# Kernel tuning notes

Hardware: AMD Instinct MI355X
Metric: run time of the kernel (lower is better)

Reference implementation:

```python
import jax, jax.numpy as jnp
import numpy as np

NLE_TERM_CO = 80
NUM_CHARS = 256
HID = 128


def setup_inputs() -> dict:
    key = jax.random.key(0)
    ks = jax.random.split(key, 9)
    B = 8192
    message = jax.random.randint(ks[0], (B, NLE_TERM_CO), 0, NUM_CHARS, dtype=jnp.int64)
    # Linear weights stored as (in, out); scaled like torch default init.
    s1 = 1.0 / np.sqrt(NLE_TERM_CO * NUM_CHARS)
    s2 = 1.0 / np.sqrt(HID)
    return {
        "message": message,
        "W1": jax.random.normal(ks[1], (NLE_TERM_CO * NUM_CHARS, HID), jnp.float32) * s1,
        "b1": jax.random.normal(ks[2], (HID,), jnp.float32) * s1,
        "W2": jax.random.normal(ks[3], (HID, HID), jnp.float32) * s2,
        "b2": jax.random.normal(ks[4], (HID,), jnp.float32) * s2,
        "W3": jax.random.normal(ks[5], (HID, HID), jnp.float32) * s2,
        "b3": jax.random.normal(ks[6], (HID,), jnp.float32) * s2,
        "W4": jax.random.normal(ks[7], (HID, HID), jnp.float32) * s2,
        "b4": jax.random.normal(ks[8], (HID,), jnp.float32) * s2,
    }


def reference(message, W1, b1, W2, b2, W3, b3, W4, b4):
    # one_hot(message) @ W1 == gather rows of W1 (viewed [pos, char, hid]) and sum over positions.
    # Exactly the same math (one-hot entries are exact 0.0/1.0 floats).
    W1r = W1.reshape(NLE_TERM_CO, NUM_CHARS, HID)
    pos = jnp.arange(NLE_TERM_CO)  # [80]
    h = W1r[pos, message]          # [B, 80, 128] gather per (position, char)
    h = jax.nn.elu(h.sum(axis=1) + b1)          # [B, 128]
    h = jax.nn.elu(h @ W2 + b2)
    h = jax.nn.elu(h @ W3 + b3)
    h = jax.nn.elu(h @ W4 + b4)
    return h
```

## Files before the change

### kernel.cpp

```cpp
#include <hip/hip_runtime.h>
#include <math.h>

#define HID  128
#define NPOS 80
#define XS   136

typedef float f4 __attribute__((ext_vector_type(4)));
typedef unsigned int u32;
typedef u32 u32x4 __attribute__((ext_vector_type(4)));
typedef __attribute__((ext_vector_type(8))) short bf16x8;
typedef __attribute__((ext_vector_type(4))) float f32x4;

__device__ __forceinline__ float elu(float x) { return x > 0.f ? x : (expf(x) - 1.f); }
__device__ __forceinline__ unsigned short f2bf(float x) {
    u32 u = __float_as_uint(x);
    return (unsigned short)((u + 0x7fffu + ((u >> 16) & 1u)) >> 16);
}
__device__ __forceinline__ float bf2f(unsigned short h) { return __uint_as_float(((u32)h) << 16); }
__device__ __forceinline__ float bflo(u32 v) { return __uint_as_float(v << 16); }
__device__ __forceinline__ float bfhi(u32 v) { return __uint_as_float(v & 0xffff0000u); }

#define W1_BLOCKS 2560
#define TR_BLOCKS 24
__global__ __launch_bounds__(256) void prep(
    const float* __restrict__ W1, const float* __restrict__ W2,
    const float* __restrict__ W3, const float* __restrict__ W4,
    unsigned short* __restrict__ W1b,
    unsigned short* __restrict__ WtH, unsigned short* __restrict__ WtL)
{
    int b = blockIdx.x;
    if (b < W1_BLOCKS) {
        int i = b * 256 + threadIdx.x;
        f4 f = ((const f4*)W1)[i];
        ushort4 u4;
        u4.x = f2bf(f.x); u4.y = f2bf(f.y); u4.z = f2bf(f.z); u4.w = f2bf(f.w);
        ((ushort4*)W1b)[i] = u4;
    } else {
        int t = (b - W1_BLOCKS) * 256 + threadIdx.x;
        int lane = t & 63;
        int q = t >> 6;
        int kt = q & 3;  q >>= 2;
        int nt = q & 1;  q >>= 1;
        int w  = q & 3;
        int L  = q >> 2;
        const float* W = (L == 0) ? W2 : (L == 1) ? W3 : W4;
        const int n    = w * 32 + nt * 16 + (lane & 15);
        const int quad = lane >> 4;
        unsigned short hs[8], ls[8];
        #pragma unroll
        for (int j = 0; j < 8; ++j) {
            const int k = kt * 32 + quad * 8 + j;
            float v = W[k * HID + n];
            hs[j] = f2bf(v);
            ls[j] = f2bf(v - bf2f(hs[j]));
        }
        *(ushort4*)&WtH[t * 8]     = make_ushort4(hs[0], hs[1], hs[2], hs[3]);
        *(ushort4*)&WtH[t * 8 + 4] = make_ushort4(hs[4], hs[5], hs[6], hs[7]);
        *(ushort4*)&WtL[t * 8]     = make_ushort4(ls[0], ls[1], ls[2], ls[3]);
        *(ushort4*)&WtL[t * 8 + 4] = make_ushort4(ls[4], ls[5], ls[6], ls[7]);
    }
}

__global__ __launch_bounds__(256) void main_k(
    const int* __restrict__ msg, const unsigned short* __restrict__ W1b,
    const float* __restrict__ b1,
    const unsigned short* __restrict__ WtH, const unsigned short* __restrict__ WtL,
    const float* __restrict__ b2, const float* __restrict__ b3,
    const float* __restrict__ b4, float* __restrict__ out)
{
    const int tid = threadIdx.x, lane = tid & 63, w = tid >> 6;
    const int quad = lane >> 4, l15 = lane & 15;
    const int m    = w * 4 + quad;
    const int soff = l15 << 3;
    const int r0   = blockIdx.x * 16;

    __shared__ int smsg[16 * NPOS];
    __shared__ unsigned short Xh[16 * XS];
    __shared__ unsigned short Xl[16 * XS];

    for (int k = tid; k < 16 * NPOS; k += 256)
        smsg[k] = msg[r0 * NPOS + k];
    __syncthreads();

    const int* mrow = &smsg[m * NPOS];
    f4 acc0 = *(const f4*)&b1[soff];
    f4 acc1 = *(const f4*)&b1[soff + 4];
    #pragma unroll 1
    for (int p0 = 0; p0 < NPOS; p0 += 8) {
        int c[8];
        #pragma unroll
        for (int u = 0; u < 8; ++u) c[u] = mrow[p0 + u];
        u32x4 v[8];
        #pragma unroll
        for (int u = 0; u < 8; ++u)
            v[u] = *(const u32x4*)&W1b[((p0 + u) << 15) + (c[u] << 7) + soff];
        #pragma unroll
        for (int u = 0; u < 8; ++u) {
            acc0.x += bflo(v[u].x); acc0.y += bfhi(v[u].x);
            acc0.z += bflo(v[u].y); acc0.w += bfhi(v[u].y);
            acc1.x += bflo(v[u].z); acc1.y += bfhi(v[u].z);
            acc1.z += bflo(v[u].w); acc1.w += bfhi(v[u].w);
        }
    }
    {
        float xs[8] = { acc0.x, acc0.y, acc0.z, acc0.w, acc1.x, acc1.y, acc1.z, acc1.w };
        unsigned short hs[8], ls[8];
        #pragma unroll
        for (int u = 0; u < 8; ++u) {
            float y = elu(xs[u]);
            hs[u] = f2bf(y);
            ls[u] = f2bf(y - bf2f(hs[u]));
        }
        *(ushort4*)&Xh[m * XS + soff]     = make_ushort4(hs[0], hs[1], hs[2], hs[3]);
        *(ushort4*)&Xh[m * XS + soff + 4] = make_ushort4(hs[4], hs[5], hs[6], hs[7]);
        *(ushort4*)&Xl[m * XS + soff]     = make_ushort4(ls[0], ls[1], ls[2], ls[3]);
        *(ushort4*)&Xl[m * XS + soff + 4] = make_ushort4(ls[4], ls[5], ls[6], ls[7]);
    }
    __syncthreads();

    const float* bs[3] = { b2, b3, b4 };
    #pragma unroll 1
    for (int L = 0; L < 3; ++L) {
        bf16x8 Ah[4], Al[4];
        #pragma unroll
        for (int kt = 0; kt < 4; ++kt) {
            const int off = l15 * XS + kt * 32 + quad * 8;
            Ah[kt] = *(const bf16x8*)&Xh[off];
            Al[kt] = *(const bf16x8*)&Xl[off];
        }
        const unsigned short* WH = WtH + L * 16384;
        const unsigned short* WL = WtL + L * 16384;
        f32x4 acc[2] = { {0,0,0,0}, {0,0,0,0} };
        #pragma unroll
        for (int nt = 0; nt < 2; ++nt) {
            #pragma unroll
            for (int kt = 0; kt < 4; ++kt) {
                const int boff = ((((w << 1) + nt) << 2) + kt) * 512 + lane * 8;
                bf16x8 Bh = *(const bf16x8*)&WH[boff];
                bf16x8 Bl = *(const bf16x8*)&WL[boff];
                acc[nt] = __builtin_amdgcn_mfma_f32_16x16x32_bf16(Ah[kt], Bh, acc[nt], 0, 0, 0);
                acc[nt] = __builtin_amdgcn_mfma_f32_16x16x32_bf16(Ah[kt], Bl, acc[nt], 0, 0, 0);
                acc[nt] = __builtin_amdgcn_mfma_f32_16x16x32_bf16(Al[kt], Bh, acc[nt], 0, 0, 0);
            }
        }
        __syncthreads();

        #pragma unroll
        for (int nt = 0; nt < 2; ++nt) {
            const int n = w * 32 + nt * 16 + l15;
            const float bias = bs[L][n];
            #pragma unroll
            for (int r = 0; r < 4; ++r) {
                const int mm = quad * 4 + r;
                const float y = elu(acc[nt][r] + bias);
                if (L < 2) {
                    unsigned short hi = f2bf(y);
                    Xh[mm * XS + n] = hi;
                    Xl[mm * XS + n] = f2bf(y - bf2f(hi));
                } else {
                    out[(r0 + mm) * HID + n] = y;
                }
            }
        }
        if (L < 2) __syncthreads();
    }
}

extern "C" void kernel_launch(void* const* d_in, const int* in_sizes, int n_in,
                              void* d_out, int out_size, void* d_ws, size_t ws_size,
                              hipStream_t stream) {
    const int*   msg = (const int*)  d_in[0];
    const float* W1  = (const float*)d_in[1];
    const float* b1  = (const float*)d_in[2];
    const float* W2  = (const float*)d_in[3];
    const float* b2  = (const float*)d_in[4];
    const float* W3  = (const float*)d_in[5];
    const float* b3  = (const float*)d_in[6];
    const float* W4  = (const float*)d_in[7];
    const float* b4  = (const float*)d_in[8];
    float* out = (float*)d_out;

    unsigned short* W1b = (unsigned short*)d_ws;
    unsigned short* WtH = W1b + 2621440;
    unsigned short* WtL = WtH + 49152;

    prep  <<<dim3(W1_BLOCKS + TR_BLOCKS), dim3(256), 0, stream>>>(W1, W2, W3, W4, W1b, WtH, WtL);
    main_k<<<dim3(512),                   dim3(256), 0, stream>>>(msg, W1b, b1, WtH, WtL,
                                                                  b2, b3, b4, out);
}
```

Baseline: 98.07 us.

## Quantize W1 to scaled FP8 e4m3 and split embedding gather across waves

```diff
diff --git a/kernel.cpp b/kernel.cpp
--- a/kernel.cpp
+++ b/kernel.cpp
@@ -6,6 +6,7 @@
 #define XS   136
 
 typedef float f4 __attribute__((ext_vector_type(4)));
+typedef float f2 __attribute__((ext_vector_type(2)));
 typedef unsigned int u32;
 typedef u32 u32x4 __attribute__((ext_vector_type(4)));
 typedef __attribute__((ext_vector_type(8))) short bf16x8;
@@ -17,24 +18,71 @@
     return (unsigned short)((u + 0x7fffu + ((u >> 16) & 1u)) >> 16);
 }
 __device__ __forceinline__ float bf2f(unsigned short h) { return __uint_as_float(((u32)h) << 16); }
-__device__ __forceinline__ float bflo(u32 v) { return __uint_as_float(v << 16); }
-__device__ __forceinline__ float bfhi(u32 v) { return __uint_as_float(v & 0xffff0000u); }
+
+__device__ __forceinline__ u32 f2e4m3(float x) {
+    u32 u = __float_as_uint(x);
+    u32 sign = (u >> 31) << 7;
+    float a = fabsf(x);
+    if (a >= 448.f) return sign | 0x7e;
+    int e = (int)((u >> 23) & 0xff) - 127;
+    if (e < -6) {
+        int q = (int)rintf(a * 512.0f);
+        if (q >= 8) return sign | 0x08;
+        return sign | (u32)q;
+    }
+    u32 sig = (u & 0x7fffffu) | 0x800000u;
+    u32 rs = sig + 0x7ffffu + ((sig >> 20) & 1u);
+    if (rs >= 0x1000000u) { e += 1; rs >>= 1; }
+    u32 m3 = (rs >> 20) & 7u;
+    u32 enc = ((u32)(e + 7) << 3) | m3;
+    if (enc >= 0x7fu) return sign | 0x7e;
+    return sign | enc;
+}
+
+#if defined(__has_builtin)
+#if __has_builtin(__builtin_amdgcn_cvt_pk_f32_fp8)
+#define HW_FP8 1
+#endif
+#endif
+
+#ifdef HW_FP8
+__device__ __forceinline__ void dec4_acc(u32 v, f4* A) {
+    f2 lo = __builtin_amdgcn_cvt_pk_f32_fp8((int)v, false);
+    f2 hi = __builtin_amdgcn_cvt_pk_f32_fp8((int)v, true);
+    (*A).x += lo.x; (*A).y += lo.y; (*A).z += hi.x; (*A).w += hi.y;
+}
+#else
+__device__ __forceinline__ float dec1(u32 b) {
+    int em = (int)(b & 0x7fu);
+    int isn = (em >= 8) ? 1 : 0;
+    int frac = (em & 7) | (isn << 3);
+    int e2 = isn ? (em >> 3) : 1;
+    float f = ldexpf((float)frac, e2 - 10);
+    return (b & 0x80u) ? -f : f;
+}
+__device__ __forceinline__ void dec4_acc(u32 v, f4* A) {
+    (*A).x += dec1(v & 0xff); (*A).y += dec1((v >> 8) & 0xff);
+    (*A).z += dec1((v >> 16) & 0xff); (*A).w += dec1(v >> 24);
+}
+#endif
 
 #define W1_BLOCKS 2560
 #define TR_BLOCKS 24
 __global__ __launch_bounds__(256) void prep(
     const float* __restrict__ W1, const float* __restrict__ W2,
     const float* __restrict__ W3, const float* __restrict__ W4,
-    unsigned short* __restrict__ W1b,
+    u32* __restrict__ W1f8,
     unsigned short* __restrict__ WtH, unsigned short* __restrict__ WtL)
 {
     int b = blockIdx.x;
     if (b < W1_BLOCKS) {
         int i = b * 256 + threadIdx.x;
         f4 f = ((const f4*)W1)[i];
-        ushort4 u4;
-        u4.x = f2bf(f.x); u4.y = f2bf(f.y); u4.z = f2bf(f.z); u4.w = f2bf(f.w);
-        ((ushort4*)W1b)[i] = u4;
+        u32 pk = f2e4m3(f.x * 64.f)
+               | (f2e4m3(f.y * 64.f) << 8)
+               | (f2e4m3(f.z * 64.f) << 16)
+               | (f2e4m3(f.w * 64.f) << 24);
+        W1f8[i] = pk;
     } else {
         int t = (b - W1_BLOCKS) * 256 + threadIdx.x;
         int lane = t & 63;
@@ -62,7 +110,7 @@
 }
 
 __global__ __launch_bounds__(256) void main_k(
-    const int* __restrict__ msg, const unsigned short* __restrict__ W1b,
+    const int* __restrict__ msg, const unsigned char* __restrict__ W1f8,
     const float* __restrict__ b1,
     const unsigned short* __restrict__ WtH, const unsigned short* __restrict__ WtL,
     const float* __restrict__ b2, const float* __restrict__ b3,
@@ -70,11 +118,10 @@
 {
     const int tid = threadIdx.x, lane = tid & 63, w = tid >> 6;
     const int quad = lane >> 4, l15 = lane & 15;
-    const int m    = w * 4 + quad;
-    const int soff = l15 << 3;
-    const int r0   = blockIdx.x * 16;
+    const int r0 = blockIdx.x * 16;
 
     __shared__ int smsg[16 * NPOS];
+    __shared__ float P[2][16][HID];
     __shared__ unsigned short Xh[16 * XS];
     __shared__ unsigned short Xl[16 * XS];
 
@@ -82,28 +129,40 @@
         smsg[k] = msg[r0 * NPOS + k];
     __syncthreads();
 
-    const int* mrow = &smsg[m * NPOS];
-    f4 acc0 = *(const f4*)&b1[soff];
-    f4 acc1 = *(const f4*)&b1[soff + 4];
-    #pragma unroll 1
-    for (int p0 = 0; p0 < NPOS; p0 += 8) {
-        int c[8];
-        #pragma unroll
-        for (int u = 0; u < 8; ++u) c[u] = mrow[p0 + u];
-        u32x4 v[8];
-        #pragma unroll
-        for (int u = 0; u < 8; ++u)
-            v[u] = *(const u32x4*)&W1b[((p0 + u) << 15) + (c[u] << 7) + soff];
-        #pragma unroll
-        for (int u = 0; u < 8; ++u) {
-            acc0.x += bflo(v[u].x); acc0.y += bfhi(v[u].x);
-            acc0.z += bflo(v[u].y); acc0.w += bfhi(v[u].y);
-            acc1.x += bflo(v[u].z); acc1.y += bfhi(v[u].z);
-            acc1.z += bflo(v[u].w); acc1.w += bfhi(v[u].w);
-        }
-    }
     {
-        float xs[8] = { acc0.x, acc0.y, acc0.z, acc0.w, acc1.x, acc1.y, acc1.z, acc1.w };
+        const int half = w >> 1;
+        const int rw   = ((w & 1) << 3) + (lane >> 3);
+        const int co   = (lane & 7) << 4;
+        const int* mr  = &smsg[rw * NPOS];
+        f4 A0 = {0,0,0,0}, A1 = {0,0,0,0}, A2 = {0,0,0,0}, A3 = {0,0,0,0};
+        const int pend = half * 40 + 40;
+        #pragma unroll 1
+        for (int p0 = half * 40; p0 < pend; p0 += 8) {
+            int c[8];
+            #pragma unroll
+            for (int u = 0; u < 8; ++u) c[u] = mr[p0 + u];
+            u32x4 v[8];
+            #pragma unroll
+            for (int u = 0; u < 8; ++u)
+                v[u] = *(const u32x4*)(W1f8 + (((p0 + u) << 15) + (c[u] << 7) + co));
+            #pragma unroll
+            for (int u = 0; u < 8; ++u) {
+                dec4_acc(v[u].x, &A0); dec4_acc(v[u].y, &A1);
+                dec4_acc(v[u].z, &A2); dec4_acc(v[u].w, &A3);
+            }
+        }
+        float* Pp = &P[half][rw][(lane & 7) << 4];
+        *(f4*)&Pp[0] = A0; *(f4*)&Pp[4] = A1; *(f4*)&Pp[8] = A2; *(f4*)&Pp[12] = A3;
+    }
+    __syncthreads();
+
+    {
+        const int m = tid >> 4, j0 = (tid & 15) << 3;
+        f4 s0 = (*(const f4*)&P[0][m][j0]     + *(const f4*)&P[1][m][j0])     * 0.015625f
+              + *(const f4*)&b1[j0];
+        f4 s1 = (*(const f4*)&P[0][m][j0 + 4] + *(const f4*)&P[1][m][j0 + 4]) * 0.015625f
+              + *(const f4*)&b1[j0 + 4];
+        float xs[8] = { s0.x, s0.y, s0.z, s0.w, s1.x, s1.y, s1.z, s1.w };
         unsigned short hs[8], ls[8];
         #pragma unroll
         for (int u = 0; u < 8; ++u) {
@@ -111,10 +170,10 @@
             hs[u] = f2bf(y);
             ls[u] = f2bf(y - bf2f(hs[u]));
         }
-        *(ushort4*)&Xh[m * XS + soff]     = make_ushort4(hs[0], hs[1], hs[2], hs[3]);
-        *(ushort4*)&Xh[m * XS + soff + 4] = make_ushort4(hs[4], hs[5], hs[6], hs[7]);
-        *(ushort4*)&Xl[m * XS + soff]     = make_ushort4(ls[0], ls[1], ls[2], ls[3]);
-        *(ushort4*)&Xl[m * XS + soff + 4] = make_ushort4(ls[4], ls[5], ls[6], ls[7]);
+        *(ushort4*)&Xh[m * XS + j0]     = make_ushort4(hs[0], hs[1], hs[2], hs[3]);
+        *(ushort4*)&Xh[m * XS + j0 + 4] = make_ushort4(hs[4], hs[5], hs[6], hs[7]);
+        *(ushort4*)&Xl[m * XS + j0]     = make_ushort4(ls[0], ls[1], ls[2], ls[3]);
+        *(ushort4*)&Xl[m * XS + j0 + 4] = make_ushort4(ls[4], ls[5], ls[6], ls[7]);
     }
     __syncthreads();
 
@@ -180,11 +239,12 @@
     const float* b4  = (const float*)d_in[8];
     float* out = (float*)d_out;
 
-    unsigned short* W1b = (unsigned short*)d_ws;
-    unsigned short* WtH = W1b + 2621440;
-    unsigned short* WtL = WtH + 49152;
-
-    prep  <<<dim3(W1_BLOCKS + TR_BLOCKS), dim3(256), 0, stream>>>(W1, W2, W3, W4, W1b, WtH, WtL);
-    main_k<<<dim3(512),                   dim3(256), 0, stream>>>(msg, W1b, b1, WtH, WtL,
+    unsigned char*  W1f8 = (unsigned char*)d_ws;
+    unsigned short* WtH  = (unsigned short*)(W1f8 + 2621440);
+    unsigned short* WtL  = WtH + 49152;
+
+    prep  <<<dim3(W1_BLOCKS + TR_BLOCKS), dim3(256), 0, stream>>>(W1, W2, W3, W4,
+                                                                  (u32*)W1f8, WtH, WtL);
+    main_k<<<dim3(512),                   dim3(256), 0, stream>>>(msg, W1f8, b1, WtH, WtL,
                                                                   b2, b3, b4, out);
 }
```

Result: no change. 96.62 us (-1.5%).
